# Performance work log

Hardware: AMD Instinct MI355X
Metric: run time of the kernel (lower is better)

Reference implementation:

```python
import jax, jax.numpy as jnp
import numpy as np

HIDDEN = 2048
VOCAB = 50257


def setup_inputs() -> dict:
    key = jax.random.key(0)
    ks = jax.random.split(key, 9)
    s = 1.0 / np.sqrt(HIDDEN)
    return {
        "input": jax.random.randint(ks[0], (1,), 0, VOCAB, dtype=jnp.int64) if jax.config.jax_enable_x64 else jax.random.randint(ks[0], (1,), 0, VOCAB, dtype=jnp.int32),
        "hidden": jax.random.normal(ks[1], (1, 1, HIDDEN), dtype=jnp.float32),
        "embedding": jax.random.normal(ks[2], (VOCAB, HIDDEN), dtype=jnp.float32),
        "w_ih": jax.random.uniform(ks[3], (3 * HIDDEN, HIDDEN), jnp.float32, -s, s),
        "w_hh": jax.random.uniform(ks[4], (3 * HIDDEN, HIDDEN), jnp.float32, -s, s),
        "b_ih": jax.random.uniform(ks[5], (3 * HIDDEN,), jnp.float32, -s, s),
        "b_hh": jax.random.uniform(ks[6], (3 * HIDDEN,), jnp.float32, -s, s),
        "out_w": jax.random.uniform(ks[7], (VOCAB, HIDDEN), jnp.float32, -s, s),
        "out_b": jax.random.uniform(ks[8], (VOCAB,), jnp.float32, -s, s),
    }


def reference(input, hidden, embedding, w_ih, w_hh, b_ih, b_hh, out_w, out_b):
    # embedding lookup + view(1,1,-1) + relu  -> x: [H]
    x = jax.nn.relu(embedding[input[0]])
    h = hidden[0, 0]  # [H]
    # PyTorch GRU single step: gates ordered (r, z, n)
    gi = w_ih @ x + b_ih  # [3H]
    gh = w_hh @ h + b_hh  # [3H]
    i_r, i_z, i_n = jnp.split(gi, 3)
    h_r, h_z, h_n = jnp.split(gh, 3)
    r = jax.nn.sigmoid(i_r + h_r)
    z = jax.nn.sigmoid(i_z + h_z)
    n = jnp.tanh(i_n + r * h_n)
    h_new = (1.0 - z) * n + z * h  # [H]
    # output projection (nn.Linear: x @ W.T + b) + log_softmax(dim=1)
    logits = out_w @ h_new + out_b  # [V]
    logp = jax.nn.log_softmax(logits)[None, :]  # [1, V]
    return logp, h_new[None, None, :]
```

## Files before the change

kernel.cpp:

```cpp
#include <hip/hip_runtime.h>
#include <math.h>

#define H 2048
#define V 50257

#define LOGITS_BLOCKS 2048
#define LOGITS_WAVES (LOGITS_BLOCKS * 4)
#define FIN_BLOCKS 52

__device__ __forceinline__ float wave_reduce_sum(float v) {
#pragma unroll
    for (int off = 32; off > 0; off >>= 1)
        v += __shfl_down(v, off, 64);
    return v;
}

__global__ __launch_bounds__(384) void k_gru(
    const int* __restrict__ idx_p, const float* __restrict__ emb,
    const float* __restrict__ hid,
    const float* __restrict__ w_ih, const float* __restrict__ w_hh,
    const float* __restrict__ b_ih, const float* __restrict__ b_hh,
    float* __restrict__ hnew_ws, float* __restrict__ hnew_out) {
    __shared__ float xs[H];
    __shared__ float hs[H];
    __shared__ float partial[6][2];
    int tid = threadIdx.x;

    long idx = (long)idx_p[0];
    const float4* embrow = (const float4*)(emb + idx * (long)H);
    for (int i = tid; i < H / 4; i += 384) {
        float4 e = embrow[i];
        e.x = fmaxf(e.x, 0.f); e.y = fmaxf(e.y, 0.f);
        e.z = fmaxf(e.z, 0.f); e.w = fmaxf(e.w, 0.f);
        ((float4*)xs)[i] = e;
        ((float4*)hs)[i] = ((const float4*)hid)[i];
    }
    __syncthreads();

    int wid = tid >> 6, lane = tid & 63;
    int gate = wid % 3;
    const float* W   = (wid < 3) ? w_ih : w_hh;
    const float* vec = (wid < 3) ? xs : hs;
    int j0 = blockIdx.x, j1 = blockIdx.x + 1024;
    const float4* r0 = (const float4*)(W + ((size_t)gate * H + j0) * (size_t)H);
    const float4* r1 = (const float4*)(W + ((size_t)gate * H + j1) * (size_t)H);

    float4 vreg[8];
#pragma unroll
    for (int it = 0; it < 8; ++it)
        vreg[it] = ((const float4*)vec)[it * 64 + lane];

    float a0 = 0.f, a1 = 0.f;
#pragma unroll
    for (int it = 0; it < 8; ++it) {
        float4 wa = r0[it * 64 + lane];
        float4 wb = r1[it * 64 + lane];
        a0 += wa.x * vreg[it].x + wa.y * vreg[it].y + wa.z * vreg[it].z + wa.w * vreg[it].w;
        a1 += wb.x * vreg[it].x + wb.y * vreg[it].y + wb.z * vreg[it].z + wb.w * vreg[it].w;
    }
    a0 = wave_reduce_sum(a0);
    a1 = wave_reduce_sum(a1);
    if (lane == 0) { partial[wid][0] = a0; partial[wid][1] = a1; }
    __syncthreads();

    if (tid < 2) {
        int j = (tid == 0) ? j0 : j1;
        float i_r = partial[0][tid] + b_ih[j];
        float i_z = partial[1][tid] + b_ih[H + j];
        float i_n = partial[2][tid] + b_ih[2 * H + j];
        float h_r = partial[3][tid] + b_hh[j];
        float h_z = partial[4][tid] + b_hh[H + j];
        float h_n = partial[5][tid] + b_hh[2 * H + j];
        float r = 1.f / (1.f + expf(-(i_r + h_r)));
        float z = 1.f / (1.f + expf(-(i_z + h_z)));
        float n = tanhf(i_n + r * h_n);
        float hv = (1.f - z) * n + z * hs[j];
        hnew_ws[j] = hv;
        hnew_out[j] = hv;
    }
}

__global__ __launch_bounds__(256, 4) void k_logits(
    const float* __restrict__ out_w, const float* __restrict__ out_b,
    const float* __restrict__ hnew,
    float* __restrict__ out, float2* __restrict__ partials) {
    __shared__ float hsm[H];
    __shared__ float pm[4], ps[4];
    int tid = threadIdx.x;
    for (int i = tid; i < H / 4; i += 256)
        ((float4*)hsm)[i] = ((const float4*)hnew)[i];
    __syncthreads();

    int wid = tid >> 6, lane = tid & 63;
    const int gw = blockIdx.x * 4 + wid;
    float4 vreg[8];
#pragma unroll
    for (int it = 0; it < 8; ++it)
        vreg[it] = ((const float4*)hsm)[it * 64 + lane];

    float m = -INFINITY, s = 0.f;
#pragma unroll 1
    for (int t = 0; t < 3; ++t) {
        int r0 = gw + t * 16384;
        int r1 = r0 + 8192;
        const float4* row0 = (const float4*)(out_w + (size_t)r0 * H);
        const float4* row1 = (const float4*)(out_w + (size_t)r1 * H);
        float a0 = 0.f, a1 = 0.f;
#pragma unroll
        for (int it = 0; it < 8; ++it) {
            float4 wa = row0[it * 64 + lane];
            float4 wb = row1[it * 64 + lane];
            a0 += wa.x * vreg[it].x + wa.y * vreg[it].y + wa.z * vreg[it].z + wa.w * vreg[it].w;
            a1 += wb.x * vreg[it].x + wb.y * vreg[it].y + wb.z * vreg[it].z + wb.w * vreg[it].w;
        }
        a0 = wave_reduce_sum(a0);
        a1 = wave_reduce_sum(a1);
        if (lane == 0) {
            float l0 = a0 + out_b[r0], l1 = a1 + out_b[r1];
            out[r0] = l0; out[r1] = l1;
            float M = fmaxf(m, fmaxf(l0, l1));
            s = s * __expf(m - M) + __expf(l0 - M) + __expf(l1 - M);
            m = M;
        }
    }
    if (gw < V - 49152) {
        int r = 49152 + gw;
        const float4* row = (const float4*)(out_w + (size_t)r * H);
        float a0 = 0.f;
#pragma unroll
        for (int it = 0; it < 8; ++it) {
            float4 wa = row[it * 64 + lane];
            a0 += wa.x * vreg[it].x + wa.y * vreg[it].y + wa.z * vreg[it].z + wa.w * vreg[it].w;
        }
        a0 = wave_reduce_sum(a0);
        if (lane == 0) {
            float l = a0 + out_b[r];
            out[r] = l;
            float M = fmaxf(m, l);
            s = s * __expf(m - M) + __expf(l - M);
            m = M;
        }
    }
    if (lane == 0) { pm[wid] = m; ps[wid] = s; }
    __syncthreads();
    if (tid == 0) {
        float M = fmaxf(fmaxf(pm[0], pm[1]), fmaxf(pm[2], pm[3]));
        float S = ps[0] * __expf(pm[0] - M) + ps[1] * __expf(pm[1] - M) +
                  ps[2] * __expf(pm[2] - M) + ps[3] * __expf(pm[3] - M);
        partials[blockIdx.x] = make_float2(M, S);
    }
}

__global__ __launch_bounds__(256) void k_finalize(
    const float2* __restrict__ partials, float* __restrict__ out) {
    __shared__ float pm[4], ps[4];
    __shared__ float cs;
    int tid = threadIdx.x;

    float m = -INFINITY, s = 0.f;
    for (int i = tid; i < LOGITS_BLOCKS; i += 256) {
        float2 p = partials[i];
        float M = fmaxf(m, p.x);
        s = s * __expf(m - M) + p.y * __expf(p.x - M);
        m = M;
    }
#pragma unroll
    for (int off = 32; off > 0; off >>= 1) {
        float om = __shfl_down(m, off, 64);
        float os = __shfl_down(s, off, 64);
        float M = fmaxf(m, om);
        s = s * __expf(m - M) + os * __expf(om - M);
        m = M;
    }
    int wid = tid >> 6, lane = tid & 63;
    if (lane == 0) { pm[wid] = m; ps[wid] = s; }
    __syncthreads();
    if (tid == 0) {
        float M = fmaxf(fmaxf(pm[0], pm[1]), fmaxf(pm[2], pm[3]));
        float S = ps[0] * __expf(pm[0] - M) + ps[1] * __expf(pm[1] - M) +
                  ps[2] * __expf(pm[2] - M) + ps[3] * __expf(pm[3] - M);
        cs = M + logf(S);
    }
    __syncthreads();
    float C = cs;

    int gid = blockIdx.x * 256 + tid;
    const int nf = V / 4;
    for (int i = gid; i < nf; i += FIN_BLOCKS * 256) {
        float4 l4 = ((const float4*)out)[i];
        l4.x -= C; l4.y -= C; l4.z -= C; l4.w -= C;
        ((float4*)out)[i] = l4;
    }
    if (gid == 0) out[V - 1] -= C;
}

extern "C" void kernel_launch(void* const* d_in, const int* in_sizes, int n_in,
                              void* d_out, int out_size, void* d_ws, size_t ws_size,
                              hipStream_t stream) {
    const int*   idx    = (const int*)d_in[0];
    const float* hidden = (const float*)d_in[1];
    const float* emb    = (const float*)d_in[2];
    const float* w_ih   = (const float*)d_in[3];
    const float* w_hh   = (const float*)d_in[4];
    const float* b_ih   = (const float*)d_in[5];
    const float* b_hh   = (const float*)d_in[6];
    const float* out_w  = (const float*)d_in[7];
    const float* out_b  = (const float*)d_in[8];

    float* out = (float*)d_out;
    float* ws  = (float*)d_ws;
    float*  hnew     = ws;
    float2* partials = (float2*)(ws + H);

    k_gru<<<1024, 384, 0, stream>>>(idx, emb, hidden, w_ih, w_hh, b_ih, b_hh,
                                    hnew, out + V);
    k_logits<<<LOGITS_BLOCKS, 256, 0, stream>>>(out_w, out_b, hnew, out, partials);
    k_finalize<<<FIN_BLOCKS, 256, 0, stream>>>(partials, out);
}
```

Before: 100.9 us.

## Fuse logits and log-softmax finalize via grid barrier, keep logits in LDS

Merges the finalize kernel into the logits kernel using an atomic-counter grid barrier across 1024 persistent blocks. Each wave keeps its 13 logits in shared memory and writes them once, already normalised, instead of writing raw logits and re-reading them in a separate pass. This removes one kernel launch and one read-modify-write pass over the output. The cost is a software grid-wide spin barrier whose correctness depends on all 1024 blocks being resident at once.

```diff
diff --git a/kernel.cpp b/kernel.cpp
--- a/kernel.cpp
+++ b/kernel.cpp
@@ -3,16 +3,22 @@
 
 #define H 2048
 #define V 50257
-
-#define LOGITS_BLOCKS 2048
-#define LOGITS_WAVES (LOGITS_BLOCKS * 4)
-#define FIN_BLOCKS 52
+#define NTHR 256
+#define LB 1024
+
+typedef unsigned long long u64;
 
 __device__ __forceinline__ float wave_reduce_sum(float v) {
 #pragma unroll
     for (int off = 32; off > 0; off >>= 1)
         v += __shfl_down(v, off, 64);
     return v;
+}
+
+__device__ __forceinline__ void online_comb(float& m, float& s, float om, float os) {
+    float M = fmaxf(m, om);
+    s = s * __expf(m - M) + os * __expf(om - M);
+    m = M;
 }
 
 __global__ __launch_bounds__(384) void k_gru(
@@ -20,11 +26,14 @@
     const float* __restrict__ hid,
     const float* __restrict__ w_ih, const float* __restrict__ w_hh,
     const float* __restrict__ b_ih, const float* __restrict__ b_hh,
-    float* __restrict__ hnew_ws, float* __restrict__ hnew_out) {
+    float* __restrict__ hnew_ws, float* __restrict__ hnew_out,
+    unsigned int* __restrict__ counter) {
     __shared__ float xs[H];
     __shared__ float hs[H];
     __shared__ float partial[6][2];
     int tid = threadIdx.x;
+
+    if (blockIdx.x == 0 && tid == 0) *counter = 0;
 
     long idx = (long)idx_p[0];
     const float4* embrow = (const float4*)(emb + idx * (long)H);
@@ -80,19 +89,21 @@
     }
 }
 
-__global__ __launch_bounds__(256, 4) void k_logits(
+__global__ __launch_bounds__(NTHR, 4) void k_logits_fused(
     const float* __restrict__ out_w, const float* __restrict__ out_b,
-    const float* __restrict__ hnew,
-    float* __restrict__ out, float2* __restrict__ partials) {
+    const float* __restrict__ hnew, float* __restrict__ out,
+    u64* __restrict__ partials, unsigned int* __restrict__ counter) {
     __shared__ float hsm[H];
+    __shared__ float l_lds[4][13];
     __shared__ float pm[4], ps[4];
-    int tid = threadIdx.x;
-    for (int i = tid; i < H / 4; i += 256)
+    __shared__ float c_s;
+    const int tid = threadIdx.x, wid = tid >> 6, lane = tid & 63;
+    const int gw = blockIdx.x * 4 + wid;
+
+    for (int i = tid; i < H / 4; i += NTHR)
         ((float4*)hsm)[i] = ((const float4*)hnew)[i];
     __syncthreads();
 
-    int wid = tid >> 6, lane = tid & 63;
-    const int gw = blockIdx.x * 4 + wid;
     float4 vreg[8];
 #pragma unroll
     for (int it = 0; it < 8; ++it)
@@ -100,9 +111,9 @@
 
     float m = -INFINITY, s = 0.f;
 #pragma unroll 1
-    for (int t = 0; t < 3; ++t) {
-        int r0 = gw + t * 16384;
-        int r1 = r0 + 8192;
+    for (int k = 0; k < 6; ++k) {
+        int r0 = gw + (2 * k) * 4096;
+        int r1 = r0 + 4096;
         const float4* row0 = (const float4*)(out_w + (size_t)r0 * H);
         const float4* row1 = (const float4*)(out_w + (size_t)r1 * H);
         float a0 = 0.f, a1 = 0.f;
@@ -117,13 +128,14 @@
         a1 = wave_reduce_sum(a1);
         if (lane == 0) {
             float l0 = a0 + out_b[r0], l1 = a1 + out_b[r1];
-            out[r0] = l0; out[r1] = l1;
-            float M = fmaxf(m, fmaxf(l0, l1));
-            s = s * __expf(m - M) + __expf(l0 - M) + __expf(l1 - M);
-            m = M;
-        }
-    }
-    if (gw < V - 49152) {
+            l_lds[wid][2 * k]     = l0;
+            l_lds[wid][2 * k + 1] = l1;
+            online_comb(m, s, l0, 1.0f);
+            online_comb(m, s, l1, 1.0f);
+        }
+    }
+    const bool has_tail = gw < (V - 49152);
+    if (has_tail) {
         int r = 49152 + gw;
         const float4* row = (const float4*)(out_w + (size_t)r * H);
         float a0 = 0.f;
@@ -135,63 +147,60 @@
         a0 = wave_reduce_sum(a0);
         if (lane == 0) {
             float l = a0 + out_b[r];
-            out[r] = l;
-            float M = fmaxf(m, l);
-            s = s * __expf(m - M) + __expf(l - M);
-            m = M;
+            l_lds[wid][12] = l;
+            online_comb(m, s, l, 1.0f);
         }
     }
     if (lane == 0) { pm[wid] = m; ps[wid] = s; }
     __syncthreads();
+
     if (tid == 0) {
-        float M = fmaxf(fmaxf(pm[0], pm[1]), fmaxf(pm[2], pm[3]));
-        float S = ps[0] * __expf(pm[0] - M) + ps[1] * __expf(pm[1] - M) +
-                  ps[2] * __expf(pm[2] - M) + ps[3] * __expf(pm[3] - M);
-        partials[blockIdx.x] = make_float2(M, S);
-    }
-}
-
-__global__ __launch_bounds__(256) void k_finalize(
-    const float2* __restrict__ partials, float* __restrict__ out) {
-    __shared__ float pm[4], ps[4];
-    __shared__ float cs;
-    int tid = threadIdx.x;
-
-    float m = -INFINITY, s = 0.f;
-    for (int i = tid; i < LOGITS_BLOCKS; i += 256) {
-        float2 p = partials[i];
-        float M = fmaxf(m, p.x);
-        s = s * __expf(m - M) + p.y * __expf(p.x - M);
-        m = M;
+        float M = pm[0], S = ps[0];
+        online_comb(M, S, pm[1], ps[1]);
+        online_comb(M, S, pm[2], ps[2]);
+        online_comb(M, S, pm[3], ps[3]);
+        u64 pk = ((u64)__float_as_uint(S) << 32) | (u64)__float_as_uint(M);
+        __hip_atomic_store(&partials[blockIdx.x], pk, __ATOMIC_RELAXED,
+                           __HIP_MEMORY_SCOPE_AGENT);
+        __hip_atomic_fetch_add(counter, 1u, __ATOMIC_RELEASE,
+                               __HIP_MEMORY_SCOPE_AGENT);
+        while (__hip_atomic_load(counter, __ATOMIC_ACQUIRE,
+                                 __HIP_MEMORY_SCOPE_AGENT) < LB)
+            __builtin_amdgcn_s_sleep(16);
+    }
+    __syncthreads();
+
+    float mm = -INFINITY, ss = 0.f;
+    for (int i = tid; i < LB; i += NTHR) {
+        u64 pk = __hip_atomic_load(&partials[i], __ATOMIC_RELAXED,
+                                   __HIP_MEMORY_SCOPE_AGENT);
+        float pmv = __uint_as_float((unsigned)(pk & 0xffffffffu));
+        float psv = __uint_as_float((unsigned)(pk >> 32));
+        online_comb(mm, ss, pmv, psv);
     }
 #pragma unroll
     for (int off = 32; off > 0; off >>= 1) {
-        float om = __shfl_down(m, off, 64);
-        float os = __shfl_down(s, off, 64);
-        float M = fmaxf(m, om);
-        s = s * __expf(m - M) + os * __expf(om - M);
-        m = M;
-    }
-    int wid = tid >> 6, lane = tid & 63;
-    if (lane == 0) { pm[wid] = m; ps[wid] = s; }
+        float om = __shfl_down(mm, off, 64);
+        float os = __shfl_down(ss, off, 64);
+        online_comb(mm, ss, om, os);
+    }
+    if (lane == 0) { pm[wid] = mm; ps[wid] = ss; }
     __syncthreads();
     if (tid == 0) {
-        float M = fmaxf(fmaxf(pm[0], pm[1]), fmaxf(pm[2], pm[3]));
-        float S = ps[0] * __expf(pm[0] - M) + ps[1] * __expf(pm[1] - M) +
-                  ps[2] * __expf(pm[2] - M) + ps[3] * __expf(pm[3] - M);
-        cs = M + logf(S);
-    }
-    __syncthreads();
-    float C = cs;
-
-    int gid = blockIdx.x * 256 + tid;
-    const int nf = V / 4;
-    for (int i = gid; i < nf; i += FIN_BLOCKS * 256) {
-        float4 l4 = ((const float4*)out)[i];
-        l4.x -= C; l4.y -= C; l4.z -= C; l4.w -= C;
-        ((float4*)out)[i] = l4;
-    }
-    if (gid == 0) out[V - 1] -= C;
+        float M = pm[0], S = ps[0];
+        online_comb(M, S, pm[1], ps[1]);
+        online_comb(M, S, pm[2], ps[2]);
+        online_comb(M, S, pm[3], ps[3]);
+        c_s = M + logf(S);
+    }
+    __syncthreads();
+    const float C = c_s;
+
+    if (lane < 12) {
+        out[gw + lane * 4096] = l_lds[wid][lane] - C;
+    } else if (lane == 12 && has_tail) {
+        out[49152 + gw] = l_lds[wid][12] - C;
+    }
 }
 
 extern "C" void kernel_launch(void* const* d_in, const int* in_sizes, int n_in,
@@ -209,11 +218,12 @@
 
     float* out = (float*)d_out;
     float* ws  = (float*)d_ws;
-    float*  hnew     = ws;
-    float2* partials = (float2*)(ws + H);
+    float*        hnew     = ws;
+    u64*          partials = (u64*)(ws + H);
+    unsigned int* counter  = (unsigned int*)(ws + H + 2 * LB);
 
     k_gru<<<1024, 384, 0, stream>>>(idx, emb, hidden, w_ih, w_hh, b_ih, b_hh,
-                                    hnew, out + V);
-    k_logits<<<LOGITS_BLOCKS, 256, 0, stream>>>(out_w, out_b, hnew, out, partials);
-    k_finalize<<<FIN_BLOCKS, 256, 0, stream>>>(partials, out);
-}
+                                    hnew, out + V, counter);
+    k_logits_fused<<<LB, NTHR, 0, stream>>>(out_w, out_b, hnew, out,
+                                            partials, counter);
+}
```

Result: slower. 210.2 us (+108.3%).
